# Optimization experiments

Hardware: AMD Instinct MI355X
Metric: run time of the kernel (lower is better)

The kernel has to match this reference:

```python
import jax, jax.numpy as jnp
import numpy as np

NUM_EXPERTS = 8
TOP_K = 2
D_MODEL = 1024
D_FF = 4096
TOKENS = 8192


def setup_inputs() -> dict:
    key = jax.random.key(0)
    ks = jax.random.split(key, 7)
    s_in = 1.0 / np.sqrt(D_MODEL)
    s_ff = 1.0 / np.sqrt(D_FF)
    return {
        "x": jax.random.normal(ks[0], (TOKENS, D_MODEL), dtype=jnp.float32),
        "gate_w": jax.random.normal(ks[1], (D_MODEL, NUM_EXPERTS), dtype=jnp.float32) * s_in,
        "gate_b": jnp.zeros((NUM_EXPERTS,), dtype=jnp.float32),
        "w1": jax.random.normal(ks[2], (NUM_EXPERTS, D_MODEL, D_FF), dtype=jnp.float32) * s_in,
        "b1": jnp.zeros((NUM_EXPERTS, D_FF), dtype=jnp.float32),
        "w2": jax.random.normal(ks[3], (NUM_EXPERTS, D_FF, D_MODEL), dtype=jnp.float32) * s_ff,
        "b2": jnp.zeros((NUM_EXPERTS, D_MODEL), dtype=jnp.float32),
    }


def reference(x, gate_w, gate_b, w1, b1, w2, b2):
    # gate: softmax over experts, then top-k routing
    probs = jax.nn.softmax(x @ gate_w + gate_b, axis=-1)  # [T, E]
    topk_p, topk_i = jax.lax.top_k(probs, TOP_K)          # [T, K]
    T, E = probs.shape
    # dense per-token combine weights: zero for unrouted experts
    comb = jnp.zeros((T, E), dtype=x.dtype).at[jnp.arange(T)[:, None], topk_i].set(topk_p)
    out = jnp.zeros_like(x)
    for e in range(E):  # small fixed expert loop; math identical to masked gather/scatter
        h = jax.nn.silu(x @ w1[e] + b1[e])                # [T, D_FF]
        out = out + comb[:, e:e + 1] * (h @ w2[e] + b2[e])
    return out
```

## Files before the change

### kernel.cpp

```cpp
#include <hip/hip_runtime.h>
#include <hip/hip_bf16.h>
#include <math.h>

#define TOKENS 8192
#define DMODEL 1024
#define DFF    4096
#define NEXP   8
#define ESTRIDE   8448
#define MAX_SLOTS 72
#define BK 64

typedef __bf16 bf16;
typedef bf16  bf16x4 __attribute__((ext_vector_type(4)));
typedef bf16  bf16x8 __attribute__((ext_vector_type(8)));
typedef float f32x4  __attribute__((ext_vector_type(4)));

__device__ __forceinline__ void gload16(const bf16* g, bf16* l) {
    __builtin_amdgcn_global_load_lds(
        (const __attribute__((address_space(1))) void*)g,
        (__attribute__((address_space(3))) void*)l,
        16, 0, 0);
}

__global__ __launch_bounds__(256) void gate_kernel(
    const float* __restrict__ x, const float* __restrict__ gw, const float* __restrict__ gb,
    int2* __restrict__ topk_i, float2* __restrict__ topk_p, bf16* __restrict__ xb)
{
    int wid  = (blockIdx.x * blockDim.x + threadIdx.x) >> 6;
    int lane = threadIdx.x & 63;
    if (wid >= TOKENS) return;
    const float* xr = x + (size_t)wid * DMODEL;
    bf16* xbr = xb + (size_t)wid * DMODEL;
    float a0=0,a1=0,a2=0,a3=0,a4=0,a5=0,a6=0,a7=0;
    #pragma unroll
    for (int i = 0; i < 4; ++i) {
        int cq = i*256 + lane*4;
        float4 xv = *(const float4*)(xr + cq);
        bf16x4 xc = { (bf16)xv.x, (bf16)xv.y, (bf16)xv.z, (bf16)xv.w };
        *(bf16x4*)(xbr + cq) = xc;
        #pragma unroll
        for (int j = 0; j < 4; ++j) {
            float xe = (j==0)?xv.x:(j==1)?xv.y:(j==2)?xv.z:xv.w;
            const float4* g = (const float4*)(gw + (size_t)(cq + j) * NEXP);
            float4 g0 = g[0], g1 = g[1];
            a0 += xe * g0.x; a1 += xe * g0.y; a2 += xe * g0.z; a3 += xe * g0.w;
            a4 += xe * g1.x; a5 += xe * g1.y; a6 += xe * g1.z; a7 += xe * g1.w;
        }
    }
    #pragma unroll
    for (int off = 32; off; off >>= 1) {
        a0 += __shfl_xor(a0, off); a1 += __shfl_xor(a1, off);
        a2 += __shfl_xor(a2, off); a3 += __shfl_xor(a3, off);
        a4 += __shfl_xor(a4, off); a5 += __shfl_xor(a5, off);
        a6 += __shfl_xor(a6, off); a7 += __shfl_xor(a7, off);
    }
    if (lane == 0) {
        float l[NEXP] = { a0+gb[0], a1+gb[1], a2+gb[2], a3+gb[3],
                          a4+gb[4], a5+gb[5], a6+gb[6], a7+gb[7] };
        float m = l[0];
        #pragma unroll
        for (int e = 1; e < NEXP; ++e) m = fmaxf(m, l[e]);
        float p[NEXP], s = 0.f;
        #pragma unroll
        for (int e = 0; e < NEXP; ++e) { p[e] = expf(l[e] - m); s += p[e]; }
        float inv = 1.0f / s;
        int i1 = 0; float b1v = p[0];
        #pragma unroll
        for (int e = 1; e < NEXP; ++e) if (p[e] > b1v) { b1v = p[e]; i1 = e; }
        int i2 = -1; float b2v = -1.f;
        #pragma unroll
        for (int e = 0; e < NEXP; ++e) if (e != i1 && p[e] > b2v) { b2v = p[e]; i2 = e; }
        topk_i[wid] = make_int2(i1, i2);
        topk_p[wid] = make_float2(b1v * inv, b2v * inv);
    }
}

__global__ __launch_bounds__(64) void compact_kernel(
    const int2* __restrict__ topk_i, const float2* __restrict__ topk_p,
    int* __restrict__ counts, int* __restrict__ token_ids, float* __restrict__ pair_p)
{
    int e = blockIdx.x;
    int lane = threadIdx.x;
    int base = 0;
    for (int it = 0; it < TOKENS/64; ++it) {
        int t = it*64 + lane;
        int2 ki = topk_i[t];
        bool hit = (ki.x == e) || (ki.y == e);
        int which = (ki.y == e) ? 1 : 0;
        unsigned long long m = __ballot(hit);
        if (hit) {
            int idx = base + __popcll(m & ((1ull << lane) - 1ull));
            float2 kp = topk_p[t];
            token_ids[e*ESTRIDE + idx] = t | (which << 13);
            pair_p   [e*ESTRIDE + idx] = which ? kp.y : kp.x;
        }
        base += __popcll(m);
    }
    if (lane == 0) counts[e] = base;
}

__global__ void build_slots(const int* __restrict__ counts, int* n_slots,
                            int* slot_e, int* slot_row0, int* slot_gbase)
{
    __shared__ int sc[8], spb[9], stb[9];
    int t = threadIdx.x;
    if (t < 8) sc[t] = counts[t];
    __syncthreads();
    if (t == 0) {
        int pb = 0, tb = 0;
        for (int e = 0; e < NEXP; ++e) {
            spb[e] = pb; stb[e] = tb;
            pb += ((sc[e] + 127) >> 7) << 7;
            tb += (sc[e] + 255) >> 8;
        }
        spb[8] = pb; stb[8] = tb;
        *n_slots = tb;
    }
    __syncthreads();
    if (t < stb[8]) { int e = 0; while (t >= stb[e+1]) ++e;
        slot_e[t] = e; slot_row0[t] = (t - stb[e]) << 8; slot_gbase[t] = spb[e]; }
}

__global__ __launch_bounds__(256) void transpose_cvt(
    const float* __restrict__ src, bf16* __restrict__ dst, int R, int C)
{
    __shared__ bf16 tile[64 * 72];
    int e = blockIdx.z;
    int c0 = blockIdx.x * 64, r0 = blockIdx.y * 64;
    const float* s = src + (size_t)e * R * C;
    bf16* d = dst + (size_t)e * R * C;
    int t = threadIdx.x;
    {
        int r = t >> 2, q = t & 3;
        const float4* sp = (const float4*)(s + (size_t)(r0 + r) * C + c0 + q * 16);
        float4 v0 = sp[0], v1 = sp[1], v2 = sp[2], v3 = sp[3];
        bf16x8 p0, p1;
        p0[0]=(bf16)v0.x; p0[1]=(bf16)v0.y; p0[2]=(bf16)v0.z; p0[3]=(bf16)v0.w;
        p0[4]=(bf16)v1.x; p0[5]=(bf16)v1.y; p0[6]=(bf16)v1.z; p0[7]=(bf16)v1.w;
        p1[0]=(bf16)v2.x; p1[1]=(bf16)v2.y; p1[2]=(bf16)v2.z; p1[3]=(bf16)v2.w;
        p1[4]=(bf16)v3.x; p1[5]=(bf16)v3.y; p1[6]=(bf16)v3.z; p1[7]=(bf16)v3.w;
        bf16* w = tile + r * 72 + (q ^ (r >> 4)) * 16;
        *(bf16x8*)w = p0; *(bf16x8*)(w + 8) = p1;
    }
    __syncthreads();
    {
        int c = t >> 2, rq = t & 3;
        int gc = c >> 4, cl = c & 15;
        bf16x8 q0, q1;
        #pragma unroll
        for (int k = 0; k < 8; ++k) {
            q0[k] = tile[(rq*16 + k) * 72 + (gc ^ rq) * 16 + cl];
            q1[k] = tile[(rq*16 + 8 + k) * 72 + (gc ^ rq) * 16 + cl];
        }
        bf16* dp = d + (size_t)(c0 + c) * R + r0 + rq * 16;
        *(bf16x8*)dp = q0;
        *(bf16x8*)(dp + 8) = q1;
    }
}

__global__ __launch_bounds__(512, 2) void moe_gemm1(
    const bf16* __restrict__ Xb, const bf16* __restrict__ Bt,
    const float* __restrict__ bias, bf16* __restrict__ Hout,
    const int* __restrict__ token_ids,
    const int* __restrict__ slot_e, const int* __restrict__ slot_row0,
    const int* __restrict__ slot_gbase, const int* __restrict__ n_slots,
    const int* __restrict__ counts)
{
    constexpr int K = DMODEL, N = DFF, NJT = N / 256, NT = K / BK, NITER = NT / 2;

    int nwg = gridDim.x, bid = blockIdx.x;
    int wid = (bid & 7) * (nwg >> 3) + (bid >> 3);
    int slot = wid / NJT;
    if (slot >= *n_slots) return;
    int jt = wid % NJT;
    int e = slot_e[slot], row0 = slot_row0[slot], gbase = slot_gbase[slot];
    int cnt = counts[e];
    int pad_e = (cnt + 127) & ~127;
    int tlb = e * ESTRIDE;

    __shared__ __align__(16) bf16 shm[65536];

    int t = threadIdx.x, lane = t & 63, wv = t >> 6;
    int wm = wv >> 2, wn = wv & 3;
    int lr = lane & 15, kq = lane >> 4;
    int bh = wn >> 1, bro = (wn & 1) * 64;

    int aoff[2][2]; int boff[2][2];
    const bf16* Bbase = Bt + (size_t)e * N * K;
    int g8 = ((lane & 7) ^ (lane >> 3)) * 8;
    #pragma unroll
    for (int h = 0; h < 2; ++h)
        #pragma unroll
        for (int q = 0; q < 2; ++q) {
            int rloc = h*128 + wv*16 + q*8 + (lane >> 3);
            int tok = token_ids[tlb + row0 + rloc] & 0x1FFF;
            aoff[h][q] = tok * DMODEL + g8;
            boff[h][q] = (jt*256 + rloc) * K + g8;
        }

    f32x4 acc[8][4] = {};
    bf16x8 breg[4][2];

    #define STAGE_A(S, H, T) do { int _t = ((T) < NT ? (T) : 0) * BK;                   \
        gload16(Xb + aoff[H][0] + _t, shm + (((S)*2+(H))*128 + wv*16    ) * BK);        \
        gload16(Xb + aoff[H][1] + _t, shm + (((S)*2+(H))*128 + wv*16 + 8) * BK); } while(0)
    #define STAGE_B(S, H, T) do { int _t = ((T) < NT ? (T) : 0) * BK;                           \
        gload16(Bbase + boff[H][0] + _t, shm + 32768 + (((S)*2+(H))*128 + wv*16    ) * BK);     \
        gload16(Bbase + boff[H][1] + _t, shm + 32768 + (((S)*2+(H))*128 + wv*16 + 8) * BK); } while(0)

    STAGE_A(0,0,0); STAGE_A(0,1,0); STAGE_B(0,0,0); STAGE_B(0,1,0);
    STAGE_B(1,0,1); STAGE_B(1,1,1);
    asm volatile("s_waitcnt vmcnt(4)" ::: "memory");
    __builtin_amdgcn_s_barrier();

    #define LOAD_A(S, Q)                                                             \
        _Pragma("unroll") for (int mi = 0; mi < 2; ++mi)                             \
            _Pragma("unroll") for (int kk = 0; kk < 2; ++kk)                         \
                areg[mi][kk] = *(const bf16x8*)(shm +                                \
                    (((S)*2+wm)*128 + ((Q)*2+mi)*16 + lr) * BK +                     \
                    ((kk*4+kq) ^ (lr & 7)) * 8);
    #define MFMA_Q(Q)                                                                \
        __builtin_amdgcn_s_setprio(1);                                               \
        _Pragma("unroll") for (int mi = 0; mi < 2; ++mi)                             \
            _Pragma("unroll") for (int n = 0; n < 4; ++n)                            \
                _Pragma("unroll") for (int kk = 0; kk < 2; ++kk)                     \
                    acc[(Q)*2+mi][n] = __builtin_amdgcn_mfma_f32_16x16x32_bf16(      \
                        areg[mi][kk], breg[n][kk], acc[(Q)*2+mi][n], 0, 0, 0);       \
        __builtin_amdgcn_s_setprio(0);

    #define PHASE2(S, Q2, STAGE_CODE, DO_WAIT)                                       \
    {                                                                                \
        bf16x8 areg[2][2];                                                           \
        if ((Q2) == 0) {                                                             \
            _Pragma("unroll") for (int n = 0; n < 4; ++n)                            \
                _Pragma("unroll") for (int kk = 0; kk < 2; ++kk)                     \
                    breg[n][kk] = *(const bf16x8*)(shm + 32768 +                     \
                        (((S)*2+bh)*128 + bro + n*16 + lr) * BK +                    \
                        ((kk*4+kq) ^ (lr & 7)) * 8);                                 \
        }                                                                            \
        LOAD_A(S, (Q2)*2)                                                            \
        STAGE_CODE;                                                                  \
        asm volatile("" ::: "memory");                                               \
        __builtin_amdgcn_s_barrier();                                                \
        MFMA_Q((Q2)*2)                                                               \
        LOAD_A(S, (Q2)*2+1)                                                          \
        MFMA_Q((Q2)*2+1)                                                             \
        if (DO_WAIT) asm volatile("s_waitcnt vmcnt(4)" ::: "memory");                \
        asm volatile("" ::: "memory");                                               \
        __builtin_amdgcn_s_barrier();                                                \
    }

    for (int i = 0; i < NITER; ++i) {
        int TO = 2*i+1, TE2 = 2*i+2, TO2 = 2*i+3;
        PHASE2(0, 0, { STAGE_A(1,0,TO);  STAGE_A(1,1,TO);  }, 0)
        PHASE2(0, 1, { STAGE_B(0,0,TE2); STAGE_B(0,1,TE2); }, 1)
        PHASE2(1, 0, { STAGE_A(0,0,TE2); STAGE_A(0,1,TE2); }, 0)
        PHASE2(1, 1, { STAGE_B(1,0,TO2); STAGE_B(1,1,TO2); }, 1)
    }
    asm volatile("s_waitcnt vmcnt(0)" ::: "memory");
    #undef PHASE2
    #undef MFMA_Q
    #undef LOAD_A
    #undef STAGE_A
    #undef STAGE_B

    int lro = kq * 4;
    float bv[4];
    #pragma unroll
    for (int n = 0; n < 4; ++n)
        bv[n] = bias[e * DFF + jt*256 + wn*64 + n*16 + lr];
    #pragma unroll
    for (int m = 0; m < 8; ++m)
        #pragma unroll
        for (int reg = 0; reg < 4; ++reg) {
            int rl = wm*128 + m*16 + lro + reg;
            if (row0 + rl < pad_e) {
                size_t hrow = (size_t)(gbase + row0 + rl);
                #pragma unroll
                for (int n = 0; n < 4; ++n) {
                    int col = jt*256 + wn*64 + n*16 + lr;
                    float v = acc[m][n][reg] + bv[n];
                    v = v / (1.0f + __expf(-v));
                    __builtin_nontemporal_store((bf16)v, &Hout[hrow * DFF + col]);
                }
            }
        }
}

__global__ __launch_bounds__(512, 2) void moe_gemm2(
    const bf16* __restrict__ Ah, const bf16* __restrict__ Bt,
    const float* __restrict__ bias, float* __restrict__ pbuf,
    const int* __restrict__ token_ids, const float* __restrict__ pair_p,
    const int* __restrict__ slot_e, const int* __restrict__ slot_row0,
    const int* __restrict__ slot_gbase, const int* __restrict__ n_slots,
    const int* __restrict__ counts)
{
    constexpr int K = DFF, N = DMODEL, NJT = N / 128, NT = K / BK;

    int nwg = gridDim.x, bid = blockIdx.x;
    int wid = (bid & 7) * (nwg >> 3) + (bid >> 3);
    int slot = wid / NJT;
    if (slot >= *n_slots) return;
    int jt = wid % NJT;
    int e = slot_e[slot], row0 = slot_row0[slot], gbase = slot_gbase[slot];
    int cnt = counts[e];
    int tlb = e * ESTRIDE;

    __shared__ __align__(16) bf16 shm[73728];

    int t = threadIdx.x, lane = t & 63, wv = t >> 6;
    int wm4 = wv >> 1, wn2 = wv & 1;
    int lr = lane & 15, kq = lane >> 4;
    int g8 = ((lane & 7) ^ (lane >> 3)) * 8;

    int aoff[4], boff[2];
    const bf16* Bbase = Bt + (size_t)e * N * K;
    #pragma unroll
    for (int q = 0; q < 4; ++q) {
        int rloc = wv*32 + q*8 + (lane >> 3);
        aoff[q] = (gbase + row0 + rloc) * DFF + g8;
    }
    #pragma unroll
    for (int q = 0; q < 2; ++q) {
        int rloc = wv*16 + q*8 + (lane >> 3);
        boff[q] = (jt*128 + rloc) * K + g8;
    }

    f32x4 acc[4][4] = {};

    #define ST2(S, T) do { int _t = ((T) < NT ? (T) : 0) * BK;                        \
        _Pragma("unroll") for (int q = 0; q < 4; ++q)                                 \
            gload16(Ah + aoff[q] + _t, shm + (S)*16384 + (wv*32 + q*8)*BK);           \
        _Pragma("unroll") for (int q = 0; q < 2; ++q)                                 \
            gload16(Bbase + boff[q] + _t, shm + 49152 + (S)*8192 + (wv*16 + q*8)*BK); \
        } while (0)

    ST2(0, 0); ST2(1, 1);
    int cs = 0, ps = 2;
    for (int tt = 0; tt < NT; ++tt) {
        ST2(ps, tt + 2);
        asm volatile("s_waitcnt vmcnt(12)" ::: "memory");
        __builtin_amdgcn_s_barrier();
        bf16x8 areg[4][2], breg[4][2];
        #pragma unroll
        for (int m = 0; m < 4; ++m)
            #pragma unroll
            for (int kk = 0; kk < 2; ++kk)
                areg[m][kk] = *(const bf16x8*)(shm + cs*16384 +
                    (wm4*64 + m*16 + lr)*BK + ((kk*4+kq) ^ (lr & 7))*8);
        #pragma unroll
        for (int n = 0; n < 4; ++n)
            #pragma unroll
            for (int kk = 0; kk < 2; ++kk)
                breg[n][kk] = *(const bf16x8*)(shm + 49152 + cs*8192 +
                    (wn2*64 + n*16 + lr)*BK + ((kk*4+kq) ^ (lr & 7))*8);
        __builtin_amdgcn_s_setprio(1);
        #pragma unroll
        for (int m = 0; m < 4; ++m)
            #pragma unroll
            for (int n = 0; n < 4; ++n)
                #pragma unroll
                for (int kk = 0; kk < 2; ++kk)
                    acc[m][n] = __builtin_amdgcn_mfma_f32_16x16x32_bf16(
                        areg[m][kk], breg[n][kk], acc[m][n], 0, 0, 0);
        __builtin_amdgcn_s_setprio(0);
        asm volatile("" ::: "memory");
        __builtin_amdgcn_s_barrier();
        cs = (cs == 2) ? 0 : cs + 1;
        ps = (ps == 2) ? 0 : ps + 1;
    }
    asm volatile("s_waitcnt vmcnt(0)" ::: "memory");
    #undef ST2

    float bv[4];
    #pragma unroll
    for (int n = 0; n < 4; ++n)
        bv[n] = bias[e * DMODEL + jt*128 + wn2*64 + n*16 + lr];
    #pragma unroll
    for (int m = 0; m < 4; ++m)
        #pragma unroll
        for (int reg = 0; reg < 4; ++reg) {
            int rl = wm4*64 + m*16 + kq*4 + reg;
            if (row0 + rl < cnt) {
                int pr = tlb + row0 + rl;
                int tw = token_ids[pr];
                int tok = tw & 0x1FFF, wh = (tw >> 13) & 1;
                float p = pair_p[pr];
                float* dst = pbuf + ((size_t)(tok*2 + wh)) * DMODEL;
                #pragma unroll
                for (int n = 0; n < 4; ++n) {
                    int col = jt*128 + wn2*64 + n*16 + lr;
                    __builtin_nontemporal_store(p * (acc[m][n][reg] + bv[n]), &dst[col]);
                }
            }
        }
}

__global__ __launch_bounds__(256) void combine_kernel(
    const float* __restrict__ pbuf, float* __restrict__ out)
{
    int wid  = (blockIdx.x * 256 + threadIdx.x) >> 6;
    int lane = threadIdx.x & 63;
    const f32x4* a = (const f32x4*)(pbuf + (size_t)wid * 2 * DMODEL);
    const f32x4* b = (const f32x4*)(pbuf + ((size_t)wid * 2 + 1) * DMODEL);
    f32x4* o = (f32x4*)(out + (size_t)wid * DMODEL);
    #pragma unroll
    for (int i = 0; i < 4; ++i) {
        int c = i*64 + lane;
        o[c] = a[c] + b[c];
    }
}

extern "C" void kernel_launch(void* const* d_in, const int* in_sizes, int n_in,
                              void* d_out, int out_size, void* d_ws, size_t ws_size,
                              hipStream_t stream)
{
    const float* x  = (const float*)d_in[0];
    const float* gw = (const float*)d_in[1];
    const float* gb = (const float*)d_in[2];
    const float* w1 = (const float*)d_in[3];
    const float* b1 = (const float*)d_in[4];
    const float* w2 = (const float*)d_in[5];
    const float* b2 = (const float*)d_in[6];
    float* out = (float*)d_out;

    const size_t W1T_OFF = 0;
    const size_t W2T_OFF = 67108864;
    const size_t H_OFF   = 134217728;
    const size_t S_OFF   = H_OFF + (size_t)17408 * DFF * 2;
    const size_t WS_NEEDED = S_OFF + 4096 + 2*(NEXP*ESTRIDE*4) + 2*(TOKENS*8);
    if (ws_size < WS_NEEDED) return;

    char* ws = (char*)d_ws;
    bf16*  w1t  = (bf16*)(ws + W1T_OFF);
    float* pbuf = (float*)(ws + W1T_OFF);
    bf16*  w2t  = (bf16*)(ws + W2T_OFF);
    bf16*  xb   = (bf16*)(ws + W2T_OFF);
    bf16*  h    = (bf16*)(ws + H_OFF);
    char*  S    = ws + S_OFF;
    int*   counts    = (int*)(S + 0);
    int*   n_slots   = (int*)(S + 64);
    int*   slot_e    = (int*)(S + 128);
    int*   slot_row0 = (int*)(S + 512);
    int*   slot_gbase= (int*)(S + 896);
    int*   token_ids = (int*)(S + 4096);
    float* pair_p    = (float*)(S + 4096 + NEXP*ESTRIDE*4);
    int2*  topk_i    = (int2*)(S + 4096 + 2*(NEXP*ESTRIDE*4));
    float2* topk_p   = (float2*)(S + 4096 + 2*(NEXP*ESTRIDE*4) + TOKENS*8);

    transpose_cvt<<<dim3(DFF/64, DMODEL/64, NEXP), dim3(256), 0, stream>>>(w1, w1t, DMODEL, DFF);

    gate_kernel<<<TOKENS * 64 / 256, 256, 0, stream>>>(x, gw, gb, topk_i, topk_p, xb);
    compact_kernel<<<NEXP, 64, 0, stream>>>(topk_i, topk_p, counts, token_ids, pair_p);
    build_slots<<<1, 128, 0, stream>>>(counts, n_slots, slot_e, slot_row0, slot_gbase);

    moe_gemm1<<<MAX_SLOTS * (DFF/256), 512, 0, stream>>>(
        xb, w1t, b1, h, token_ids, slot_e, slot_row0, slot_gbase, n_slots, counts);

    transpose_cvt<<<dim3(DMODEL/64, DFF/64, NEXP), dim3(256), 0, stream>>>(w2, w2t, DFF, DMODEL);

    moe_gemm2<<<MAX_SLOTS * (DMODEL/128), 512, 0, stream>>>(
        h, w2t, b2, pbuf, token_ids, pair_p, slot_e, slot_row0, slot_gbase, n_slots, counts);

    combine_kernel<<<TOKENS * 64 / 256, 256, 0, stream>>>(pbuf, out);
}
```

Baseline: 591.7 us.

## Split gemm2 K dimension in two and store bf16 partials for combine

The second expert GEMM is split along the DFF reduction into two halves, doubling the workgroup count so more of the GPU is busy when the slot count is small. Each half writes a separate bf16 partial (bias added only by the first half), and the combine kernel sums four bf16 partials per token in fp32. Partial traffic stays about the same size as before, because there are twice as many partials at half the width. The cost is extra rounding error from storing the partials in bf16.

```diff
diff --git a/kernel.cpp b/kernel.cpp
--- a/kernel.cpp
+++ b/kernel.cpp
@@ -289,19 +289,22 @@
 
 __global__ __launch_bounds__(512, 2) void moe_gemm2(
     const bf16* __restrict__ Ah, const bf16* __restrict__ Bt,
-    const float* __restrict__ bias, float* __restrict__ pbuf,
+    const float* __restrict__ bias, bf16* __restrict__ pbuf,
     const int* __restrict__ token_ids, const float* __restrict__ pair_p,
     const int* __restrict__ slot_e, const int* __restrict__ slot_row0,
     const int* __restrict__ slot_gbase, const int* __restrict__ n_slots,
     const int* __restrict__ counts)
 {
-    constexpr int K = DFF, N = DMODEL, NJT = N / 128, NT = K / BK;
+    constexpr int K = DFF, N = DMODEL, NJT = N / 128;
+    constexpr int KSPL = 2, KCH = K / KSPL, NT = KCH / BK;
 
     int nwg = gridDim.x, bid = blockIdx.x;
     int wid = (bid & 7) * (nwg >> 3) + (bid >> 3);
-    int slot = wid / NJT;
+    int slot = wid / (NJT * KSPL);
     if (slot >= *n_slots) return;
-    int jt = wid % NJT;
+    int rem = wid % (NJT * KSPL);
+    int jt = rem / KSPL, split = rem % KSPL;
+    int kbase = split * KCH;
     int e = slot_e[slot], row0 = slot_row0[slot], gbase = slot_gbase[slot];
     int cnt = counts[e];
     int tlb = e * ESTRIDE;
@@ -318,12 +321,12 @@
     #pragma unroll
     for (int q = 0; q < 4; ++q) {
         int rloc = wv*32 + q*8 + (lane >> 3);
-        aoff[q] = (gbase + row0 + rloc) * DFF + g8;
+        aoff[q] = (gbase + row0 + rloc) * DFF + kbase + g8;
     }
     #pragma unroll
     for (int q = 0; q < 2; ++q) {
         int rloc = wv*16 + q*8 + (lane >> 3);
-        boff[q] = (jt*128 + rloc) * K + g8;
+        boff[q] = (jt*128 + rloc) * K + kbase + g8;
     }
 
     f32x4 acc[4][4] = {};
@@ -375,7 +378,7 @@
     float bv[4];
     #pragma unroll
     for (int n = 0; n < 4; ++n)
-        bv[n] = bias[e * DMODEL + jt*128 + wn2*64 + n*16 + lr];
+        bv[n] = (split == 0) ? bias[e * DMODEL + jt*128 + wn2*64 + n*16 + lr] : 0.0f;
     #pragma unroll
     for (int m = 0; m < 4; ++m)
         #pragma unroll
@@ -386,28 +389,39 @@
                 int tw = token_ids[pr];
                 int tok = tw & 0x1FFF, wh = (tw >> 13) & 1;
                 float p = pair_p[pr];
-                float* dst = pbuf + ((size_t)(tok*2 + wh)) * DMODEL;
+                bf16* dst = pbuf + ((size_t)(tok*4 + wh*2 + split)) * DMODEL;
                 #pragma unroll
                 for (int n = 0; n < 4; ++n) {
                     int col = jt*128 + wn2*64 + n*16 + lr;
-                    __builtin_nontemporal_store(p * (acc[m][n][reg] + bv[n]), &dst[col]);
+                    __builtin_nontemporal_store((bf16)(p * (acc[m][n][reg] + bv[n])), &dst[col]);
                 }
             }
         }
 }
 
 __global__ __launch_bounds__(256) void combine_kernel(
-    const float* __restrict__ pbuf, float* __restrict__ out)
+    const bf16* __restrict__ pbuf, float* __restrict__ out)
 {
     int wid  = (blockIdx.x * 256 + threadIdx.x) >> 6;
     int lane = threadIdx.x & 63;
-    const f32x4* a = (const f32x4*)(pbuf + (size_t)wid * 2 * DMODEL);
-    const f32x4* b = (const f32x4*)(pbuf + ((size_t)wid * 2 + 1) * DMODEL);
-    f32x4* o = (f32x4*)(out + (size_t)wid * DMODEL);
-    #pragma unroll
-    for (int i = 0; i < 4; ++i) {
-        int c = i*64 + lane;
-        o[c] = a[c] + b[c];
+    const bf16* pr = pbuf + (size_t)wid * 4 * DMODEL;
+    float* o = out + (size_t)wid * DMODEL;
+    #pragma unroll
+    for (int i = 0; i < 2; ++i) {
+        int c = (i*64 + lane) * 8;
+        bf16x8 v0 = *(const bf16x8*)(pr + c);
+        bf16x8 v1 = *(const bf16x8*)(pr + DMODEL + c);
+        bf16x8 v2 = *(const bf16x8*)(pr + 2*DMODEL + c);
+        bf16x8 v3 = *(const bf16x8*)(pr + 3*DMODEL + c);
+        f32x4 r0, r1;
+        #pragma unroll
+        for (int k = 0; k < 4; ++k)
+            r0[k] = (float)v0[k] + (float)v1[k] + (float)v2[k] + (float)v3[k];
+        #pragma unroll
+        for (int k = 0; k < 4; ++k)
+            r1[k] = (float)v0[4+k] + (float)v1[4+k] + (float)v2[4+k] + (float)v3[4+k];
+        *(f32x4*)(o + c) = r0;
+        *(f32x4*)(o + c + 4) = r1;
     }
 }
 
@@ -433,7 +447,7 @@
 
     char* ws = (char*)d_ws;
     bf16*  w1t  = (bf16*)(ws + W1T_OFF);
-    float* pbuf = (float*)(ws + W1T_OFF);
+    bf16*  pbuf = (bf16*)(ws + W1T_OFF);
     bf16*  w2t  = (bf16*)(ws + W2T_OFF);
     bf16*  xb   = (bf16*)(ws + W2T_OFF);
     bf16*  h    = (bf16*)(ws + H_OFF);
@@ -459,7 +473,7 @@
 
     transpose_cvt<<<dim3(DMODEL/64, DFF/64, NEXP), dim3(256), 0, stream>>>(w2, w2t, DFF, DMODEL);
 
-    moe_gemm2<<<MAX_SLOTS * (DMODEL/128), 512, 0, stream>>>(
+    moe_gemm2<<<MAX_SLOTS * (DMODEL/128) * 2, 512, 0, stream>>>(
         h, w2t, b2, pbuf, token_ids, pair_p, slot_e, slot_row0, slot_gbase, n_slots, counts);
 
     combine_kernel<<<TOKENS * 64 / 256, 256, 0, stream>>>(pbuf, out);
```

Result: faster. 577.6 us, median of 2 (-2.4%).
